# Kernel optimization log

Measured on AMD Instinct MI355X. Metric: run time of the kernel, lower is better.

The kernel has to match this reference:

```python
import jax, jax.numpy as jnp
import numpy as np


def setup_inputs() -> dict:
    key = jax.random.key(0)
    k1, k2 = jax.random.split(key)
    x = jax.random.normal(k1, (8, 2048, 1024), dtype=jnp.float32)
    codebooks = jax.random.normal(k2, (8, 2048, 128), dtype=jnp.float32)
    return {"x": x, "codebooks": codebooks}


def reference(x, codebooks):
    # x: [b, n, h*d]; codebooks: [h, m, d]
    b, n, f = x.shape
    h, m, d = codebooks.shape
    q = x.reshape(b, n, h, d).transpose(0, 2, 1, 3)  # [b, h, n, d]
    # squared L2 distance: ||q||^2 + ||c||^2 - 2 q.c
    l2_q = jnp.sum(q * q, axis=-1, keepdims=True)          # [b, h, n, 1]
    l2_c = jnp.sum(codebooks * codebooks, axis=-1)          # [h, m]
    sim = jnp.einsum('bhnd,hmd->bhnm', q, codebooks)        # [b, h, n, m]
    dist = l2_q + l2_c[None, :, None, :] - 2.0 * sim
    idx = jnp.argmin(dist, axis=-1)                          # [b, h, n]
    # direct gather instead of one-hot @ codebook (same math)
    quant = codebooks[jnp.arange(h)[None, :, None], idx]     # [b, h, n, d]
    quant = quant.transpose(0, 2, 1, 3).reshape(b, n, f)
    # straight-through estimator (training-mode forward)
    out = x + jax.lax.stop_gradient(quant - x)
    return out
```

## Files before the change

### kernel.cpp

```cpp
#include <hip/hip_runtime.h>
#include <stddef.h>
#include <stdint.h>


#define NHEAD  8
#define NCODE  2048
#define DDIM   128
#define NQTOT  16384
#define BQ     128
#define CCH    64
#define NCHUNK (NCODE / CCH)
#define CHB    (CCH * DDIM * 2)
#define TAU    0.05f
#define WS_NEED (8u*1024u*1024u + 64u*1024u)

typedef __attribute__((ext_vector_type(8))) short short8;
typedef __attribute__((ext_vector_type(4))) float f32x4;

__device__ __forceinline__ unsigned short f2bf(float f) {
  unsigned u = __builtin_bit_cast(unsigned, f);
  u = u + 0x7fffu + ((u >> 16) & 1u);
  return (unsigned short)(u >> 16);
}
__device__ __forceinline__ float bf2f(unsigned short s) {
  unsigned u = ((unsigned)s) << 16;
  return __builtin_bit_cast(float, u);
}

__global__ __launch_bounds__(256) void vq_prep(const float* __restrict__ cb,
                                               unsigned char* __restrict__ ws)
{
  unsigned short* hi_img = (unsigned short*)ws;
  unsigned short* lo_img = (unsigned short*)(ws + 4u*1024u*1024u);
  float* cn = (float*)(ws + 8u*1024u*1024u);

  const int tg   = blockIdx.x * 256 + threadIdx.x;
  const int rg   = tg >> 4;
  const int slot = tg & 15;
  const int m    = rg & (NCODE - 1);
  const int rowc = m & 63;
  const int srcslot = slot ^ (rowc & 7);

  const float* src = cb + (size_t)rg * DDIM + srcslot * 8;
  float4 a = *(const float4*)(src);
  float4 b = *(const float4*)(src + 4);
  float f[8] = {a.x, a.y, a.z, a.w, b.x, b.y, b.z, b.w};
  short8 hv, lv;
  float nrm = 0.f;
#pragma unroll
  for (int j = 0; j < 8; ++j) {
    float v = f[j];
    nrm = fmaf(v, v, nrm);
    unsigned short hh = f2bf(v);
    float r = v - bf2f(hh);
    hv[j] = (short)hh;
    lv[j] = (short)f2bf(r);
  }
  size_t off = ((size_t)(rg >> 6) * 16384 + rowc * 256 + slot * 16) / 2;
  *(short8*)(hi_img + off) = hv;
  *(short8*)(lo_img + off) = lv;
#pragma unroll
  for (int msk = 1; msk < 16; msk <<= 1) nrm += __shfl_xor(nrm, msk);
  if (slot == 0) cn[rg] = 0.5f * nrm;
}

__global__ __launch_bounds__(256) void vq_main(const float* __restrict__ x,
                                               const float* __restrict__ cb,
                                               const unsigned char* __restrict__ ws,
                                               float* __restrict__ out)
{
  __shared__ __align__(16) unsigned char Ct[2][2 * CHB];
  __shared__ int   fidx[BQ];
  __shared__ int   flaglist[BQ];
  __shared__ int   nflag;
  __shared__ float qrow[DDIM];
  __shared__ float redS[4];
  __shared__ int   redI[4];

  const int tid  = threadIdx.x;
  const int w    = tid >> 6, l = tid & 63;
  const int lrow = l & 15,  lg = l >> 4;
  const int h    = blockIdx.y;
  const int qbase = blockIdx.x * BQ;

  const unsigned char* hi_img = ws;
  const unsigned char* lo_img = ws + 4u*1024u*1024u;
  const float* cnh = (const float*)(ws + 8u*1024u*1024u) + h * NCODE;
  const float* cbh = cb + (size_t)h * NCODE * DDIM;

  if (tid == 0) nflag = 0;

  short8 Ah[2][4], Al[2][4];
#pragma unroll
  for (int rf = 0; rf < 2; ++rf)
#pragma unroll
    for (int ks = 0; ks < 4; ++ks) {
      const float* p = x + (size_t)(qbase + w*32 + rf*16 + lrow) * 1024
                         + h * DDIM + ks * 32 + lg * 8;
      float4 a = *(const float4*)p;
      float4 b = *(const float4*)(p + 4);
      float f[8] = {a.x, a.y, a.z, a.w, b.x, b.y, b.z, b.w};
#pragma unroll
      for (int j = 0; j < 8; ++j) {
        unsigned short hh = f2bf(f[j]);
        Ah[rf][ks][j] = (short)hh;
        Al[rf][ks][j] = (short)f2bf(f[j] - bf2f(hh));
      }
    }

  float best[8], sec[8];
  int   bidx[8];
#pragma unroll
  for (int i = 0; i < 8; ++i) { best[i] = 3.4e38f; sec[i] = 3.4e38f; bidx[i] = 0; }

  const size_t himgbase = (size_t)h * 32 * 16384;
  auto STAGE = [&](int buf, int c) {
    const unsigned char* gh = hi_img + himgbase + (size_t)c * 16384;
    const unsigned char* gl = lo_img + himgbase + (size_t)c * 16384;
    unsigned char* lb = &Ct[buf][0];
#pragma unroll
    for (int r = 0; r < 4; ++r) {
      const int sub = (r * 4 + w) * 1024;
      __builtin_amdgcn_global_load_lds(
          (const __attribute__((address_space(1))) void*)(gh + sub + l * 16),
          (__attribute__((address_space(3))) void*)(lb + sub), 16, 0, 0);
    }
#pragma unroll
    for (int r = 0; r < 4; ++r) {
      const int sub = (r * 4 + w) * 1024;
      __builtin_amdgcn_global_load_lds(
          (const __attribute__((address_space(1))) void*)(gl + sub + l * 16),
          (__attribute__((address_space(3))) void*)(lb + CHB + sub), 16, 0, 0);
    }
  };

  STAGE(0, 0);
  __syncthreads();

  int cur = 0;
  for (int c = 0; c < NCHUNK; ++c) {
    if (c + 1 < NCHUNK) STAGE(cur ^ 1, c + 1);

    const int cbase = c * CCH;
    float cnv[4];
#pragma unroll
    for (int cf = 0; cf < 4; ++cf) cnv[cf] = cnh[cbase + cf * 16 + lrow];

    f32x4 acc[2][4];
#pragma unroll
    for (int rf = 0; rf < 2; ++rf)
#pragma unroll
      for (int cf = 0; cf < 4; ++cf) acc[rf][cf] = (f32x4){0.f, 0.f, 0.f, 0.f};

    const unsigned char* lb = &Ct[cur][0];
#pragma unroll
    for (int ks = 0; ks < 4; ++ks) {
#pragma unroll
      for (int cf = 0; cf < 4; ++cf) {
        const int row  = cf * 16 + lrow;
        const int boff = row * 256 + (((ks * 4 + lg) ^ (row & 7)) * 16);
        short8 bh  = *(const short8*)(lb + boff);
        short8 blo = *(const short8*)(lb + CHB + boff);
#pragma unroll
        for (int rf = 0; rf < 2; ++rf) {
          acc[rf][cf] = __builtin_amdgcn_mfma_f32_16x16x32_bf16(Ah[rf][ks], bh,  acc[rf][cf], 0, 0, 0);
          acc[rf][cf] = __builtin_amdgcn_mfma_f32_16x16x32_bf16(Al[rf][ks], bh,  acc[rf][cf], 0, 0, 0);
          acc[rf][cf] = __builtin_amdgcn_mfma_f32_16x16x32_bf16(Ah[rf][ks], blo, acc[rf][cf], 0, 0, 0);
        }
      }
    }

#pragma unroll
    for (int cf = 0; cf < 4; ++cf) {
      const int m0 = cbase + cf * 16 + lrow;
#pragma unroll
      for (int rf = 0; rf < 2; ++rf)
#pragma unroll
        for (int r = 0; r < 4; ++r) {
          const float s = cnv[cf] - acc[rf][cf][r];
          const int sl = rf * 4 + r;
          if (s < best[sl]) { sec[sl] = best[sl]; best[sl] = s; bidx[sl] = m0; }
          else               sec[sl] = fminf(sec[sl], s);
        }
    }
    __syncthreads();
    cur ^= 1;
  }

#pragma unroll
  for (int msk = 1; msk < 16; msk <<= 1) {
#pragma unroll
    for (int sl = 0; sl < 8; ++sl) {
      float ob = __shfl_xor(best[sl], msk);
      float os = __shfl_xor(sec[sl],  msk);
      int   oi = __shfl_xor(bidx[sl], msk);
      bool owin = (ob < best[sl]) || (ob == best[sl] && oi < bidx[sl]);
      float lose = owin ? best[sl] : ob;
      best[sl] = owin ? ob : best[sl];
      bidx[sl] = owin ? oi : bidx[sl];
      sec[sl]  = fminf(fminf(sec[sl], os), lose);
    }
  }
  if (lrow == 0) {
#pragma unroll
    for (int sl = 0; sl < 8; ++sl) {
      const int rf = sl >> 2, r = sl & 3;
      const int qloc = w * 32 + rf * 16 + lg * 4 + r;
      fidx[qloc] = bidx[sl];
      if (sec[sl] - best[sl] < TAU) {
        int p = atomicAdd(&nflag, 1);
        flaglist[p] = qloc;
      }
    }
  }
  __syncthreads();

  const int nf = nflag;
  for (int fi = 0; fi < nf; ++fi) {
    const int qloc = flaglist[fi];
    if (tid < DDIM) qrow[tid] = x[(size_t)(qbase + qloc) * 1024 + h * DDIM + tid];
    __syncthreads();
    float bs = 3.4e38f; int bi = NCODE;
    for (int m = tid; m < NCODE; m += 256) {
      const float* cp = cbh + (size_t)m * DDIM;
      float dot = 0.f;
#pragma unroll
      for (int d = 0; d < DDIM; d += 4) {
        float4 c4 = *(const float4*)(cp + d);
        dot = fmaf(qrow[d + 0], c4.x, dot);
        dot = fmaf(qrow[d + 1], c4.y, dot);
        dot = fmaf(qrow[d + 2], c4.z, dot);
        dot = fmaf(qrow[d + 3], c4.w, dot);
      }
      const float s = cnh[m] - dot;
      if (s < bs) { bs = s; bi = m; }
    }
#pragma unroll
    for (int msk = 1; msk < 64; msk <<= 1) {
      float ob = __shfl_xor(bs, msk);
      int   oi = __shfl_xor(bi, msk);
      if (ob < bs || (ob == bs && oi < bi)) { bs = ob; bi = oi; }
    }
    if (l == 0) { redS[w] = bs; redI[w] = bi; }
    __syncthreads();
    if (tid == 0) {
      float fb = redS[0]; int fbi = redI[0];
      for (int ww = 1; ww < 4; ++ww)
        if (redS[ww] < fb || (redS[ww] == fb && redI[ww] < fbi)) { fb = redS[ww]; fbi = redI[ww]; }
      fidx[qloc] = fbi;
    }
    __syncthreads();
  }

  const int half = tid >> 7, lane = tid & 127;
  for (int r = half; r < BQ; r += 2) {
    const int m = fidx[r];
    out[(size_t)(qbase + r) * 1024 + h * DDIM + lane] = cbh[(size_t)m * DDIM + lane];
  }
}

#define FBQ  128
#define FNCH 128
#define FDK  32
#define FLDP 132

__global__ __launch_bounds__(256) void vq_argmin_fallback(
    const float* __restrict__ x, const float* __restrict__ cb, float* __restrict__ out)
{
  __shared__ float Qs[FDK][FLDP];
  __shared__ float Cs[FDK][FLDP];
  __shared__ float cnc[FNCH];
  __shared__ float redS[FBQ][16];
  __shared__ int   redI[FBQ][16];
  __shared__ int   fidx[FBQ];

  const int h = blockIdx.y, qbase = blockIdx.x * FBQ, tid = threadIdx.x;
  const int ty = tid >> 4, tx = tid & 15;
  const float* xh  = x + (size_t)qbase * 1024 + (size_t)h * DDIM;
  const float* cbh = cb + (size_t)h * NCODE * DDIM;

  float best[8]; int bidx[8];
#pragma unroll
  for (int i = 0; i < 8; ++i) { best[i] = 3.4e38f; bidx[i] = 0; }
  float acc[8][8];
#pragma unroll
  for (int i = 0; i < 8; ++i)
#pragma unroll
    for (int j = 0; j < 8; ++j) acc[i][j] = 0.f;

  const int r0 = tid >> 3, c4 = tid & 7;
  for (int mc = 0; mc < NCODE / FNCH; ++mc) {
    for (int dk = 0; dk < DDIM / FDK; ++dk) {
      __syncthreads();
#pragma unroll
      for (int p = 0; p < 4; ++p) {
        const int q = p * 32 + r0;
        float4 v = *(const float4*)(xh + (size_t)q * 1024 + dk * FDK + c4 * 4);
        Qs[c4*4+0][q] = v.x; Qs[c4*4+1][q] = v.y; Qs[c4*4+2][q] = v.z; Qs[c4*4+3][q] = v.w;
        float4 wv = *(const float4*)(cbh + (size_t)(mc*FNCH + q) * DDIM + dk * FDK + c4 * 4);
        Cs[c4*4+0][q] = wv.x; Cs[c4*4+1][q] = wv.y; Cs[c4*4+2][q] = wv.z; Cs[c4*4+3][q] = wv.w;
      }
      __syncthreads();
#pragma unroll 8
      for (int d = 0; d < FDK; ++d) {
        float4 qa = *(const float4*)&Qs[d][ty*8];
        float4 qb = *(const float4*)&Qs[d][ty*8+4];
        float4 ca = *(const float4*)&Cs[d][tx*8];
        float4 cb4 = *(const float4*)&Cs[d][tx*8+4];
        const float qv[8] = {qa.x,qa.y,qa.z,qa.w,qb.x,qb.y,qb.z,qb.w};
        const float cv[8] = {ca.x,ca.y,ca.z,ca.w,cb4.x,cb4.y,cb4.z,cb4.w};
#pragma unroll
        for (int i = 0; i < 8; ++i)
#pragma unroll
          for (int j = 0; j < 8; ++j) acc[i][j] = fmaf(qv[i], cv[j], acc[i][j]);
      }
      if (tid < FNCH) {
        float s = 0.f;
#pragma unroll
        for (int d = 0; d < FDK; ++d) { float v = Cs[d][tid]; s = fmaf(v, v, s); }
        if (dk == 0) cnc[tid] = s; else cnc[tid] += s;
      }
    }
    __syncthreads();
#pragma unroll
    for (int j = 0; j < 8; ++j) {
      const int ml = tx * 8 + j;
      const float cn = 0.5f * cnc[ml];
      const int mg = mc * FNCH + ml;
#pragma unroll
      for (int i = 0; i < 8; ++i) {
        const float s = cn - acc[i][j];
        if (s < best[i]) { best[i] = s; bidx[i] = mg; }
        acc[i][j] = 0.f;
      }
    }
  }
#pragma unroll
  for (int i = 0; i < 8; ++i) { redS[ty*8+i][tx] = best[i]; redI[ty*8+i][tx] = bidx[i]; }
  __syncthreads();
  if (tid < FBQ) {
    float bs = redS[tid][0]; int bi = redI[tid][0];
#pragma unroll
    for (int t = 1; t < 16; ++t) {
      const float s = redS[tid][t]; const int ii = redI[tid][t];
      if (s < bs || (s == bs && ii < bi)) { bs = s; bi = ii; }
    }
    fidx[tid] = bi;
  }
  __syncthreads();
  const int half = tid >> 7, lane = tid & 127;
  for (int r = half; r < FBQ; r += 2) {
    const int m = fidx[r];
    out[(size_t)(qbase + r) * 1024 + (size_t)h * DDIM + lane] = cbh[(size_t)m * DDIM + lane];
  }
}

extern "C" void kernel_launch(void* const* d_in, const int* in_sizes, int n_in,
                              void* d_out, int out_size, void* d_ws, size_t ws_size,
                              hipStream_t stream)
{
  const float* x   = (const float*)d_in[0];
  const float* cbk = (const float*)d_in[1];
  float*       out = (float*)d_out;

  if (ws_size >= (size_t)WS_NEED) {
    vq_prep<<<dim3(1024), dim3(256), 0, stream>>>(cbk, (unsigned char*)d_ws);
    vq_main<<<dim3(NQTOT / BQ, NHEAD), dim3(256), 0, stream>>>(
        x, cbk, (const unsigned char*)d_ws, out);
  } else {
    vq_argmin_fallback<<<dim3(NQTOT / FBQ, NHEAD), dim3(256), 0, stream>>>(x, cbk, out);
  }
}
```

Baseline: 647.2 us.

## Replace split-bf16 three-pass MFMA with single fp16 MFMA pass

Swaps the hi/lo bf16 split scheme (three MFMAs per tile) for a single fp16 MFMA per tile. The codebook image and its shared-memory stage shrink to half, and the launch bounds now ask for four blocks per CU. The near-tie threshold TAU is widened so more queries get flagged for the exact fp32 recheck, which keeps argmin correct. This cuts matrix-core work and LDS/global traffic roughly threefold, at the cost of more fallback rechecks in the unseen tail code.

Result: slower. 1.833 ms (+183.1%).

```diff
diff --git a/kernel.cpp b/kernel.cpp
--- a/kernel.cpp
+++ b/kernel.cpp
@@ -11,28 +11,17 @@
 #define CCH    64
 #define NCHUNK (NCODE / CCH)
 #define CHB    (CCH * DDIM * 2)
-#define TAU    0.05f
-#define WS_NEED (8u*1024u*1024u + 64u*1024u)
-
-typedef __attribute__((ext_vector_type(8))) short short8;
+#define TAU    0.12f
+#define WS_NEED (4u*1024u*1024u + 64u*1024u)
+
+typedef __attribute__((ext_vector_type(8))) _Float16 half8;
 typedef __attribute__((ext_vector_type(4))) float f32x4;
-
-__device__ __forceinline__ unsigned short f2bf(float f) {
-  unsigned u = __builtin_bit_cast(unsigned, f);
-  u = u + 0x7fffu + ((u >> 16) & 1u);
-  return (unsigned short)(u >> 16);
-}
-__device__ __forceinline__ float bf2f(unsigned short s) {
-  unsigned u = ((unsigned)s) << 16;
-  return __builtin_bit_cast(float, u);
-}
 
 __global__ __launch_bounds__(256) void vq_prep(const float* __restrict__ cb,
                                                unsigned char* __restrict__ ws)
 {
-  unsigned short* hi_img = (unsigned short*)ws;
-  unsigned short* lo_img = (unsigned short*)(ws + 4u*1024u*1024u);
-  float* cn = (float*)(ws + 8u*1024u*1024u);
+  _Float16* img = (_Float16*)ws;
+  float* cn = (float*)(ws + 4u*1024u*1024u);
 
   const int tg   = blockIdx.x * 256 + threadIdx.x;
   const int rg   = tg >> 4;
@@ -45,31 +34,27 @@
   float4 a = *(const float4*)(src);
   float4 b = *(const float4*)(src + 4);
   float f[8] = {a.x, a.y, a.z, a.w, b.x, b.y, b.z, b.w};
-  short8 hv, lv;
+  half8 hv;
   float nrm = 0.f;
 #pragma unroll
   for (int j = 0; j < 8; ++j) {
     float v = f[j];
     nrm = fmaf(v, v, nrm);
-    unsigned short hh = f2bf(v);
-    float r = v - bf2f(hh);
-    hv[j] = (short)hh;
-    lv[j] = (short)f2bf(r);
+    hv[j] = (_Float16)v;
   }
   size_t off = ((size_t)(rg >> 6) * 16384 + rowc * 256 + slot * 16) / 2;
-  *(short8*)(hi_img + off) = hv;
-  *(short8*)(lo_img + off) = lv;
+  *(half8*)(img + off) = hv;
 #pragma unroll
   for (int msk = 1; msk < 16; msk <<= 1) nrm += __shfl_xor(nrm, msk);
   if (slot == 0) cn[rg] = 0.5f * nrm;
 }
 
-__global__ __launch_bounds__(256) void vq_main(const float* __restrict__ x,
-                                               const float* __restrict__ cb,
-                                               const unsigned char* __restrict__ ws,
-                                               float* __restrict__ out)
+__global__ __launch_bounds__(256, 4) void vq_main(const float* __restrict__ x,
+                                                  const float* __restrict__ cb,
+                                                  const unsigned char* __restrict__ ws,
+                                                  float* __restrict__ out)
 {
-  __shared__ __align__(16) unsigned char Ct[2][2 * CHB];
+  __shared__ __align__(16) unsigned char Ct[2][CHB];
   __shared__ int   fidx[BQ];
   __shared__ int   flaglist[BQ];
   __shared__ int   nflag;
@@ -83,14 +68,13 @@
   const int h    = blockIdx.y;
   const int qbase = blockIdx.x * BQ;
 
-  const unsigned char* hi_img = ws;
-  const unsigned char* lo_img = ws + 4u*1024u*1024u;
-  const float* cnh = (const float*)(ws + 8u*1024u*1024u) + h * NCODE;
+  const unsigned char* img = ws;
+  const float* cnh = (const float*)(ws + 4u*1024u*1024u) + h * NCODE;
   const float* cbh = cb + (size_t)h * NCODE * DDIM;
 
   if (tid == 0) nflag = 0;
 
-  short8 Ah[2][4], Al[2][4];
+  half8 Ah[2][4];
 #pragma unroll
   for (int rf = 0; rf < 2; ++rf)
 #pragma unroll
@@ -101,11 +85,7 @@
       float4 b = *(const float4*)(p + 4);
       float f[8] = {a.x, a.y, a.z, a.w, b.x, b.y, b.z, b.w};
 #pragma unroll
-      for (int j = 0; j < 8; ++j) {
-        unsigned short hh = f2bf(f[j]);
-        Ah[rf][ks][j] = (short)hh;
-        Al[rf][ks][j] = (short)f2bf(f[j] - bf2f(hh));
-      }
+      for (int j = 0; j < 8; ++j) Ah[rf][ks][j] = (_Float16)f[j];
     }
 
   float best[8], sec[8];
@@ -115,22 +95,14 @@
 
   const size_t himgbase = (size_t)h * 32 * 16384;
   auto STAGE = [&](int buf, int c) {
-    const unsigned char* gh = hi_img + himgbase + (size_t)c * 16384;
-    const unsigned char* gl = lo_img + himgbase + (size_t)c * 16384;
+    const unsigned char* g = img + himgbase + (size_t)c * 16384;
     unsigned char* lb = &Ct[buf][0];
 #pragma unroll
     for (int r = 0; r < 4; ++r) {
       const int sub = (r * 4 + w) * 1024;
       __builtin_amdgcn_global_load_lds(
-          (const __attribute__((address_space(1))) void*)(gh + sub + l * 16),
+          (const __attribute__((address_space(1))) void*)(g + sub + l * 16),
           (__attribute__((address_space(3))) void*)(lb + sub), 16, 0, 0);
-    }
-#pragma unroll
-    for (int r = 0; r < 4; ++r) {
-      const int sub = (r * 4 + w) * 1024;
-      __builtin_amdgcn_global_load_lds(
-          (const __attribute__((address_space(1))) void*)(gl + sub + l * 16),
-          (__attribute__((address_space(3))) void*)(lb + CHB + sub), 16, 0, 0);
     }
   };
 
@@ -159,14 +131,10 @@
       for (int cf = 0; cf < 4; ++cf) {
         const int row  = cf * 16 + lrow;
         const int boff = row * 256 + (((ks * 4 + lg) ^ (row & 7)) * 16);
-        short8 bh  = *(const short8*)(lb + boff);
-        short8 blo = *(const short8*)(lb + CHB + boff);
-#pragma unroll
-        for (int rf = 0; rf < 2; ++rf) {
-          acc[rf][cf] = __builtin_amdgcn_mfma_f32_16x16x32_bf16(Ah[rf][ks], bh,  acc[rf][cf], 0, 0, 0);
-          acc[rf][cf] = __builtin_amdgcn_mfma_f32_16x16x32_bf16(Al[rf][ks], bh,  acc[rf][cf], 0, 0, 0);
-          acc[rf][cf] = __builtin_amdgcn_mfma_f32_16x16x32_bf16(Ah[rf][ks], blo, acc[rf][cf], 0, 0, 0);
-        }
+        half8 bh = *(const half8*)(lb + boff);
+#pragma unroll
+        for (int rf = 0; rf < 2; ++rf)
+          acc[rf][cf] = __builtin_amdgcn_mfma_f32_16x16x32_f16(Ah[rf][ks], bh, acc[rf][cf], 0, 0, 0);
       }
     }
 
```
